# Kernel tuning notes

Hardware: AMD Instinct MI355X
Metric: run time of the kernel (lower is better)

## Reference

```python
import jax, jax.numpy as jnp
import numpy as np

D_MODEL = 1024
N_HEADS = 16
D_HEAD = D_MODEL // N_HEADS
LN_EPS = 1e-5


def setup_inputs() -> dict:
    key = jax.random.key(0)
    ks = jax.random.split(key, 10)
    B, N = 2, 2048
    s = 1.0 / np.sqrt(D_MODEL)
    return {
        "x": jax.random.normal(ks[0], (B, N, D_MODEL), dtype=jnp.float32),
        "Wq": jax.random.normal(ks[1], (D_MODEL, D_MODEL), dtype=jnp.float32) * s,
        "bq": jnp.zeros((D_MODEL,), dtype=jnp.float32),
        "Wk": jax.random.normal(ks[2], (D_MODEL, D_MODEL), dtype=jnp.float32) * s,
        "bk": jnp.zeros((D_MODEL,), dtype=jnp.float32),
        "Wv": jax.random.normal(ks[3], (D_MODEL, D_MODEL), dtype=jnp.float32) * s,
        "bv": jnp.zeros((D_MODEL,), dtype=jnp.float32),
        "Wo": jax.random.normal(ks[4], (D_MODEL, D_MODEL), dtype=jnp.float32) * s,
        "bo": jnp.zeros((D_MODEL,), dtype=jnp.float32),
        "ln_gamma": jnp.ones((D_MODEL,), dtype=jnp.float32),
        "ln_beta": jnp.zeros((D_MODEL,), dtype=jnp.float32),
    }


def reference(x, Wq, bq, Wk, bk, Wv, bv, Wo, bo, ln_gamma, ln_beta):
    B, N, _ = x.shape
    # QKV projections -> [B, H, N, dh]
    def proj(W, b):
        return (x @ W.T + b).reshape(B, N, N_HEADS, D_HEAD).transpose(0, 2, 1, 3)
    Q, K, V = proj(Wq, bq), proj(Wk, bk), proj(Wv, bv)
    # scaled scores [B, H, N, N] with causal mask (is_mask=True)
    scores = jnp.einsum("bhqd,bhkd->bhqk", Q, K) / np.sqrt(D_HEAD)
    causal = jnp.tril(jnp.ones((N, N), dtype=bool))
    scores = jnp.where(causal, scores, -jnp.inf)
    attn = jax.nn.softmax(scores, axis=-1)  # dropout p=0 (eval)
    ctx = jnp.einsum("bhqk,bhkd->bhqd", attn, V)  # [B, H, N, dh]
    ctx = ctx.transpose(0, 2, 1, 3).reshape(B, N, D_MODEL)
    out = ctx @ Wo.T + bo + x  # output proj + residual
    # LayerNorm over last dim
    mu = out.mean(-1, keepdims=True)
    var = out.var(-1, keepdims=True)
    return (out - mu) / jnp.sqrt(var + LN_EPS) * ln_gamma + ln_beta
```

## Files before the change

kernel.cpp:

```cpp
#include <hip/hip_runtime.h>
#include <type_traits>

#define D_MODEL 1024
#define NHEADS 16
#define DHEAD 64
#define SEQ 2048
#define BATCH 2
#define MROWS (BATCH*SEQ)
#define NQT (SEQ/64)

typedef unsigned short ushort_t;
using bf16x8 = __attribute__((ext_vector_type(8))) __bf16;
using bf16x4 = __attribute__((ext_vector_type(4))) __bf16;
using us4    = __attribute__((ext_vector_type(4))) unsigned short;
using us8    = __attribute__((ext_vector_type(8))) unsigned short;
using f32x4  = __attribute__((ext_vector_type(4))) float;

#define QSCALE 0.18033688011112042f

__device__ __forceinline__ float fast_exp2(float x) {
#if __has_builtin(__builtin_amdgcn_exp2f)
    return __builtin_amdgcn_exp2f(x);
#else
    return __expf(x * 0.6931471805599453f);
#endif
}

__device__ __forceinline__ void gl2lds(const ushort_t* g, ushort_t* l) {
    __builtin_amdgcn_global_load_lds(
        (const __attribute__((address_space(1))) unsigned int*)g,
        (__attribute__((address_space(3))) unsigned int*)l,
        16, 0, 0);
}

__global__ __launch_bounds__(256) void cvt_kernel(
    const float* __restrict__ x,
    const float* __restrict__ wq, const float* __restrict__ wk,
    const float* __restrict__ wv, const float* __restrict__ wo,
    ushort_t* __restrict__ xb,
    ushort_t* __restrict__ wqb, ushort_t* __restrict__ wkb,
    ushort_t* __restrict__ wvb, ushort_t* __restrict__ wob)
{
    const size_t XN = (size_t)MROWS * D_MODEL;
    const size_t WN = (size_t)D_MODEL * D_MODEL;
    size_t i = ((size_t)blockIdx.x * 256 + threadIdx.x) * 4;
    const float* s; ushort_t* d; size_t off;
    if (i < XN) { s = x; d = xb; off = i; }
    else {
        size_t j = i - XN;
        int w = (int)(j / WN);
        off = j - (size_t)w * WN;
        s = (w == 0) ? wq : (w == 1) ? wk : (w == 2) ? wv : wo;
        d = (w == 0) ? wqb : (w == 1) ? wkb : (w == 2) ? wvb : wob;
    }
    const f32x4 v = *(const f32x4*)(s + off);
    bf16x4 o;
    #pragma unroll
    for (int t = 0; t < 4; ++t) o[t] = (__bf16)v[t];
    *(bf16x4*)(d + off) = o;
}

template<typename OutT, bool RES>
__global__ __launch_bounds__(256, 3) void gemm_nt(
    const ushort_t* __restrict__ A,
    const ushort_t* __restrict__ W0, const ushort_t* __restrict__ W1, const ushort_t* __restrict__ W2,
    const float* __restrict__ b0, const float* __restrict__ b1, const float* __restrict__ b2,
    const float* __restrict__ res,
    OutT* __restrict__ Y0, OutT* __restrict__ Y1, OutT* __restrict__ Y2,
    float qsc)
{
    constexpr int K = D_MODEL;
    __shared__ ushort_t As[2][128 * 32];
    __shared__ ushort_t Ws[2][128 * 32];

    const int z = blockIdx.z;
    const ushort_t* W  = (z == 0) ? W0 : (z == 1) ? W1 : W2;
    const float* bias  = (z == 0) ? b0 : (z == 1) ? b1 : b2;
    OutT* Y            = (z == 0) ? Y0 : (z == 1) ? Y1 : Y2;
    const float sc     = (z == 0) ? qsc : 1.0f;

    const int i0 = blockIdx.x * 128;
    const int j0 = blockIdx.y * 128;
    const int tid  = threadIdx.x;
    const int lane = tid & 63;
    const int w    = tid >> 6;
    const int wm   = (w >> 1) * 64;
    const int wn   = (w & 1) * 64;
    const int l15  = lane & 15;
    const int quad = lane >> 4;

    const int srow = lane >> 2;
    const int scol = (lane & 3) * 8;
    const int c0 = w * 2, c1 = w * 2 + 1;
    const ushort_t* gA0 = A + (size_t)(i0 + c0 * 16 + srow) * K + scol;
    const ushort_t* gA1 = A + (size_t)(i0 + c1 * 16 + srow) * K + scol;
    const ushort_t* gW0 = W + (size_t)(j0 + c0 * 16 + srow) * K + scol;
    const ushort_t* gW1 = W + (size_t)(j0 + c1 * 16 + srow) * K + scol;

    f32x4 acc[4][4] = {};

    for (int k0 = 0; k0 < K; k0 += 64) {
        gl2lds(gA0 + k0,      &As[0][c0 * 512]);
        gl2lds(gA1 + k0,      &As[0][c1 * 512]);
        gl2lds(gA0 + k0 + 32, &As[1][c0 * 512]);
        gl2lds(gA1 + k0 + 32, &As[1][c1 * 512]);
        gl2lds(gW0 + k0,      &Ws[0][c0 * 512]);
        gl2lds(gW1 + k0,      &Ws[0][c1 * 512]);
        gl2lds(gW0 + k0 + 32, &Ws[1][c0 * 512]);
        gl2lds(gW1 + k0 + 32, &Ws[1][c1 * 512]);
        __syncthreads();

        #pragma unroll
        for (int s = 0; s < 2; ++s) {
            bf16x8 af[4], wf[4];
            #pragma unroll
            for (int m = 0; m < 4; ++m)
                af[m] = *(const bf16x8*)&As[s][(wm + m * 16 + l15) * 32 + quad * 8];
            #pragma unroll
            for (int n = 0; n < 4; ++n)
                wf[n] = *(const bf16x8*)&Ws[s][(wn + n * 16 + l15) * 32 + quad * 8];
            #pragma unroll
            for (int m = 0; m < 4; ++m)
                #pragma unroll
                for (int n = 0; n < 4; ++n)
                    acc[m][n] = __builtin_amdgcn_mfma_f32_16x16x32_bf16(wf[n], af[m], acc[m][n], 0, 0, 0);
        }
        __syncthreads();
    }

    #pragma unroll
    for (int n = 0; n < 4; ++n) {
        const int col = j0 + wn + n * 16 + quad * 4;
        const f32x4 bv = *(const f32x4*)&bias[col];
        #pragma unroll
        for (int m = 0; m < 4; ++m) {
            const int row = i0 + wm + m * 16 + l15;
            if constexpr (std::is_same<OutT, float>::value) {
                f32x4 v;
                #pragma unroll
                for (int r = 0; r < 4; ++r) v[r] = acc[m][n][r] + bv[r];
                if constexpr (RES) {
                    const f32x4 rv = *(const f32x4*)&res[(size_t)row * D_MODEL + col];
                    #pragma unroll
                    for (int r = 0; r < 4; ++r) v[r] += rv[r];
                }
                *(f32x4*)&Y[(size_t)row * D_MODEL + col] = v;
            } else {
                bf16x4 pk;
                #pragma unroll
                for (int r = 0; r < 4; ++r) pk[r] = (__bf16)((acc[m][n][r] + bv[r]) * sc);
                *(bf16x4*)&Y[(size_t)row * D_MODEL + col] = pk;
            }
        }
    }
}

#define KD 64

__device__ __forceinline__ int kswz(int row, int col) {
    return row * KD + (col ^ ((row & 7) << 3));
}

__global__ __launch_bounds__(256, 4) void attn_kernel(
    const ushort_t* __restrict__ Qg, const ushort_t* __restrict__ Kg,
    const ushort_t* __restrict__ Vg, ushort_t* __restrict__ Og)
{
    __shared__ __align__(16) ushort_t Kt[2][64 * KD];
    __shared__ __align__(16) ushort_t Vt[2][64 * KD];
    __shared__ __align__(16) ushort_t Pw[64 * KD];

    const int bh = blockIdx.x;
    const int b = bh >> 4;
    const int h = bh & 15;
    const int qt = (NQT - 1) - blockIdx.y;
    const int q0 = qt * 64;
    const int nkt = qt + 1;

    const int tid  = threadIdx.x;
    const int lane = tid & 63;
    const int w    = tid >> 6;
    const int l15  = lane & 15;
    const int quad = lane >> 4;

    const size_t headoff = (size_t)h * DHEAD;
    const ushort_t* Kbase = Kg + (size_t)(b * SEQ) * D_MODEL + headoff;
    const ushort_t* Vbase = Vg + (size_t)(b * SEQ) * D_MODEL + headoff;

    const int krow = tid >> 3;
    const int kb   = tid & 7;
    const int vkey = tid & 63;
    const int dc0  = tid >> 6;
    const int dc1  = dc0 + 4;

    const int rx = (l15 & 7) << 3;
    const int cs0 = (quad * 8) ^ rx;
    const int cs1 = (32 + quad * 8) ^ rx;
    int pwc[4];
    #pragma unroll
    for (int f = 0; f < 4; ++f) pwc[f] = (f * 16 + quad * 4) ^ rx;
    ushort_t* PwRow = &Pw[(w * 16 + l15) * KD];

    const int kwa = krow * KD + ((kb * 8) ^ ((krow & 7) << 3));

    const int qg = q0 + w * 16 + l15;
    const size_t qrow = (size_t)(b * SEQ + qg) * D_MODEL + headoff;
    const bf16x8 qf0 = *(const bf16x8*)&Qg[qrow + quad * 8];
    const bf16x8 qf1 = *(const bf16x8*)&Qg[qrow + 32 + quad * 8];

    bf16x8 onesf;
    #pragma unroll
    for (int j = 0; j < 8; ++j) onesf[j] = (__bf16)1.0f;

    float m_run = -1e30f;
    f32x4 o[4] = {};
    f32x4 o4 = {};

    us8 kp0, kp1, vp0, vp1;
    kp0 = *(const us8*)&Kbase[(size_t)krow * D_MODEL + kb * 8];
    kp1 = *(const us8*)&Kbase[(size_t)(32 + krow) * D_MODEL + kb * 8];
    vp0 = *(const us8*)&Vbase[(size_t)vkey * D_MODEL + dc0 * 8];
    vp1 = *(const us8*)&Vbase[(size_t)vkey * D_MODEL + dc1 * 8];
    *(us8*)&Kt[0][kwa]           = kp0;
    *(us8*)&Kt[0][kwa + 32 * KD] = kp1;
    #pragma unroll
    for (int j = 0; j < 8; ++j) {
        Vt[0][(dc0 * 8 + j) * KD + (vkey ^ (j << 3))] = vp0[j];
        Vt[0][(dc1 * 8 + j) * KD + (vkey ^ (j << 3))] = vp1[j];
    }
    __syncthreads();

    for (int kt = 0; kt < nkt; ++kt) {
        const int cur = kt & 1;
        const int nxt = cur ^ 1;
        const bool pre = (kt + 1 < nkt);
        if (pre) {
            const size_t koff = (size_t)((kt + 1) * 64) * D_MODEL;
            kp0 = *(const us8*)&Kbase[koff + (size_t)krow * D_MODEL + kb * 8];
            kp1 = *(const us8*)&Kbase[koff + (size_t)(32 + krow) * D_MODEL + kb * 8];
            vp0 = *(const us8*)&Vbase[koff + (size_t)vkey * D_MODEL + dc0 * 8];
            vp1 = *(const us8*)&Vbase[koff + (size_t)vkey * D_MODEL + dc1 * 8];
        }

        f32x4 sv[4];
        __builtin_amdgcn_s_setprio(1);
        #pragma unroll
        for (int f = 0; f < 4; ++f) {
            const int rbase = (f * 16 + l15) * KD;
            const bf16x8 kf0 = *(const bf16x8*)&Kt[cur][rbase + cs0];
            const bf16x8 kf1 = *(const bf16x8*)&Kt[cur][rbase + cs1];
            f32x4 s = {};
            s = __builtin_amdgcn_mfma_f32_16x16x32_bf16(kf0, qf0, s, 0, 0, 0);
            s = __builtin_amdgcn_mfma_f32_16x16x32_bf16(kf1, qf1, s, 0, 0, 0);
            sv[f] = s;
        }
        __builtin_amdgcn_s_setprio(0);

        if (kt == qt) {
            #pragma unroll
            for (int f = 0; f < 4; ++f)
                #pragma unroll
                for (int r = 0; r < 4; ++r) {
                    const int kg = kt * 64 + f * 16 + quad * 4 + r;
                    sv[f][r] = (kg <= qg) ? sv[f][r] : -1e30f;
                }
        }

        float mf[4];
        #pragma unroll
        for (int f = 0; f < 4; ++f)
            mf[f] = fmaxf(fmaxf(sv[f][0], sv[f][1]), fmaxf(sv[f][2], sv[f][3]));
        float mx = fmaxf(fmaxf(mf[0], mf[1]), fmaxf(mf[2], mf[3]));
        mx = fmaxf(mx, __shfl_xor(mx, 16));
        mx = fmaxf(mx, __shfl_xor(mx, 32));

        if (!__all(mx <= m_run + 8.0f)) {
            const float mn = fmaxf(m_run, mx);
            const float al = fast_exp2(m_run - mn);
            m_run = mn;
            #pragma unroll
            for (int t = 0; t < 4; ++t)
                #pragma unroll
                for (int r = 0; r < 4; ++r) o[t][r] *= al;
            o4[0] *= al;
        }

        #pragma unroll
        for (int f = 0; f < 4; ++f) {
            bf16x4 pk;
            #pragma unroll
            for (int r = 0; r < 4; ++r)
                pk[r] = (__bf16)fast_exp2(sv[f][r] - m_run);
            *(bf16x4*)&PwRow[pwc[f]] = pk;
        }
        __asm__ volatile("s_waitcnt lgkmcnt(0)" ::: "memory");

        __builtin_amdgcn_s_setprio(1);
        #pragma unroll
        for (int s = 0; s < 2; ++s) {
            const bf16x8 pf = *(const bf16x8*)&PwRow[s ? cs1 : cs0];
            #pragma unroll
            for (int t = 0; t < 4; ++t) {
                const bf16x8 vf = *(const bf16x8*)&Vt[cur][(t * 16 + l15) * KD + (s ? cs1 : cs0)];
                o[t] = __builtin_amdgcn_mfma_f32_16x16x32_bf16(vf, pf, o[t], 0, 0, 0);
            }
            o4 = __builtin_amdgcn_mfma_f32_16x16x32_bf16(onesf, pf, o4, 0, 0, 0);
        }
        __builtin_amdgcn_s_setprio(0);

        if (pre) {
            *(us8*)&Kt[nxt][kwa]           = kp0;
            *(us8*)&Kt[nxt][kwa + 32 * KD] = kp1;
            #pragma unroll
            for (int j = 0; j < 8; ++j) {
                Vt[nxt][(dc0 * 8 + j) * KD + (vkey ^ (j << 3))] = vp0[j];
                Vt[nxt][(dc1 * 8 + j) * KD + (vkey ^ (j << 3))] = vp1[j];
            }
        }
        __asm__ volatile("s_waitcnt lgkmcnt(0)\n\ts_barrier" ::: "memory");
    }

    const float inv = 1.f / o4[0];
    const size_t orow = (size_t)(b * SEQ + qg) * D_MODEL + headoff;
    #pragma unroll
    for (int t = 0; t < 4; ++t) {
        bf16x4 pk;
        #pragma unroll
        for (int r = 0; r < 4; ++r) pk[r] = (__bf16)(o[t][r] * inv);
        *(bf16x4*)&Og[orow + t * 16 + quad * 4] = pk;
    }
}

__global__ __launch_bounds__(256) void ln_kernel(
    const float* __restrict__ X, const float* __restrict__ g,
    const float* __restrict__ bta, float* __restrict__ out)
{
    __shared__ float r1[4], r2[4];
    const int row = blockIdx.x;
    const int tid = threadIdx.x;
    const float* p = X + (size_t)row * D_MODEL;
    float v[4]; float s1 = 0.f, s2 = 0.f;
    #pragma unroll
    for (int i = 0; i < 4; ++i) { v[i] = p[tid + 256 * i]; s1 += v[i]; s2 += v[i] * v[i]; }
    #pragma unroll
    for (int d = 32; d >= 1; d >>= 1) { s1 += __shfl_xor(s1, d); s2 += __shfl_xor(s2, d); }
    if ((tid & 63) == 0) { r1[tid >> 6] = s1; r2[tid >> 6] = s2; }
    __syncthreads();
    s1 = r1[0] + r1[1] + r1[2] + r1[3];
    s2 = r2[0] + r2[1] + r2[2] + r2[3];
    const float mu  = s1 * (1.f / D_MODEL);
    const float var = s2 * (1.f / D_MODEL) - mu * mu;
    const float rstd = rsqrtf(var + 1e-5f);
    #pragma unroll
    for (int i = 0; i < 4; ++i) {
        const int c = tid + 256 * i;
        out[(size_t)row * D_MODEL + c] = (v[i] - mu) * rstd * g[c] + bta[c];
    }
}

extern "C" void kernel_launch(void* const* d_in, const int* in_sizes, int n_in,
                              void* d_out, int out_size, void* d_ws, size_t ws_size,
                              hipStream_t stream) {
    const float* x     = (const float*)d_in[0];
    const float* Wq    = (const float*)d_in[1];
    const float* bq    = (const float*)d_in[2];
    const float* Wk    = (const float*)d_in[3];
    const float* bk    = (const float*)d_in[4];
    const float* Wv    = (const float*)d_in[5];
    const float* bv    = (const float*)d_in[6];
    const float* Wo    = (const float*)d_in[7];
    const float* bo    = (const float*)d_in[8];
    const float* gamma = (const float*)d_in[9];
    const float* beta  = (const float*)d_in[10];

    const size_t XN = (size_t)MROWS * D_MODEL;
    const size_t WN = (size_t)D_MODEL * D_MODEL;
    ushort_t* wsp = (ushort_t*)d_ws;
    ushort_t* xb  = wsp;
    ushort_t* Yq  = wsp + XN;
    ushort_t* Yk  = wsp + 2 * XN;
    ushort_t* Yv  = wsp + 3 * XN;
    ushort_t* Wqb = wsp + 4 * XN;
    ushort_t* Wkb = Wqb + WN;
    ushort_t* Wvb = Wkb + WN;
    ushort_t* Wob = Wvb + WN;
    ushort_t* ctx = xb;
    float*    pre = (float*)d_out;

    cvt_kernel<<<dim3(8192), 256, 0, stream>>>(x, Wq, Wk, Wv, Wo, xb, Wqb, Wkb, Wvb, Wob);

    gemm_nt<ushort_t, false><<<dim3(MROWS / 128, D_MODEL / 128, 3), 256, 0, stream>>>(
        xb, Wqb, Wkb, Wvb, bq, bk, bv, nullptr, Yq, Yk, Yv, QSCALE);

    attn_kernel<<<dim3(BATCH * NHEADS, NQT), 256, 0, stream>>>(Yq, Yk, Yv, ctx);

    gemm_nt<float, true><<<dim3(MROWS / 128, D_MODEL / 128, 1), 256, 0, stream>>>(
        ctx, Wob, Wob, Wob, bo, bo, bo, x, pre, pre, pre, 1.0f);

    ln_kernel<<<dim3(MROWS), 256, 0, stream>>>(pre, gamma, beta, (float*)d_out);
}
```

Measured before the change: 205.7 us.

## Vectorize V transpose stores, split P/V pipeline, and interleave causal tile order

The V tile transpose into LDS now has each thread load four 4-element rows and pack them into 64-bit stores, replacing sixteen scalar 16-bit LDS writes per thread. The softmax-exp and P·V MFMA work is split into two halves so the second half's exponentials can overlap with the first half's matrix ops. The query-tile order across blockIdx.y is interleaved, mixing long and short causal tiles to balance work across CUs. The new V layout must still match the XOR swizzle, and splitting P/V adds an extra LDS wait.

```diff
diff --git a/kernel.cpp b/kernel.cpp
--- a/kernel.cpp
+++ b/kernel.cpp
@@ -10,10 +10,12 @@
 #define NQT (SEQ/64)
 
 typedef unsigned short ushort_t;
+typedef unsigned int   u32;
 using bf16x8 = __attribute__((ext_vector_type(8))) __bf16;
 using bf16x4 = __attribute__((ext_vector_type(4))) __bf16;
 using us4    = __attribute__((ext_vector_type(4))) unsigned short;
 using us8    = __attribute__((ext_vector_type(8))) unsigned short;
+using u32x2  = __attribute__((ext_vector_type(2))) unsigned int;
 using f32x4  = __attribute__((ext_vector_type(4))) float;
 
 #define QSCALE 0.18033688011112042f
@@ -157,10 +159,6 @@
 
 #define KD 64
 
-__device__ __forceinline__ int kswz(int row, int col) {
-    return row * KD + (col ^ ((row & 7) << 3));
-}
-
 __global__ __launch_bounds__(256, 4) void attn_kernel(
     const ushort_t* __restrict__ Qg, const ushort_t* __restrict__ Kg,
     const ushort_t* __restrict__ Vg, ushort_t* __restrict__ Og)
@@ -172,7 +170,9 @@
     const int bh = blockIdx.x;
     const int b = bh >> 4;
     const int h = bh & 15;
-    const int qt = (NQT - 1) - blockIdx.y;
+    const int y = blockIdx.y;
+    const int qt = (y < 8) ? (31 - y) : (y < 16) ? (y - 8)
+                 : (y < 24) ? (39 - y) : (y - 16);
     const int q0 = qt * 64;
     const int nkt = qt + 1;
 
@@ -188,9 +188,9 @@
 
     const int krow = tid >> 3;
     const int kb   = tid & 7;
-    const int vkey = tid & 63;
-    const int dc0  = tid >> 6;
-    const int dc1  = dc0 + 4;
+
+    const int k4 = (tid & 15) * 4;
+    const int dd = (tid >> 4) * 4;
 
     const int rx = (l15 & 7) << 3;
     const int cs0 = (quad * 8) ^ rx;
@@ -215,17 +215,21 @@
     f32x4 o[4] = {};
     f32x4 o4 = {};
 
-    us8 kp0, kp1, vp0, vp1;
+    us8 kp0, kp1;
+    us4 vg[4];
     kp0 = *(const us8*)&Kbase[(size_t)krow * D_MODEL + kb * 8];
     kp1 = *(const us8*)&Kbase[(size_t)(32 + krow) * D_MODEL + kb * 8];
-    vp0 = *(const us8*)&Vbase[(size_t)vkey * D_MODEL + dc0 * 8];
-    vp1 = *(const us8*)&Vbase[(size_t)vkey * D_MODEL + dc1 * 8];
+    #pragma unroll
+    for (int j = 0; j < 4; ++j)
+        vg[j] = *(const us4*)&Vbase[(size_t)(k4 + j) * D_MODEL + dd];
     *(us8*)&Kt[0][kwa]           = kp0;
     *(us8*)&Kt[0][kwa + 32 * KD] = kp1;
     #pragma unroll
-    for (int j = 0; j < 8; ++j) {
-        Vt[0][(dc0 * 8 + j) * KD + (vkey ^ (j << 3))] = vp0[j];
-        Vt[0][(dc1 * 8 + j) * KD + (vkey ^ (j << 3))] = vp1[j];
+    for (int di = 0; di < 4; ++di) {
+        const int d = dd + di;
+        const u32 lo = (u32)vg[0][di] | ((u32)vg[1][di] << 16);
+        const u32 hi = (u32)vg[2][di] | ((u32)vg[3][di] << 16);
+        *(u32x2*)&Vt[0][d * KD + (k4 ^ ((d & 7) << 3))] = (u32x2){lo, hi};
     }
     __syncthreads();
 
@@ -237,8 +241,9 @@
             const size_t koff = (size_t)((kt + 1) * 64) * D_MODEL;
             kp0 = *(const us8*)&Kbase[koff + (size_t)krow * D_MODEL + kb * 8];
             kp1 = *(const us8*)&Kbase[koff + (size_t)(32 + krow) * D_MODEL + kb * 8];
-            vp0 = *(const us8*)&Vbase[koff + (size_t)vkey * D_MODEL + dc0 * 8];
-            vp1 = *(const us8*)&Vbase[koff + (size_t)vkey * D_MODEL + dc1 * 8];
+            #pragma unroll
+            for (int j = 0; j < 4; ++j)
+                vg[j] = *(const us4*)&Vbase[koff + (size_t)(k4 + j) * D_MODEL + dd];
         }
 
         f32x4 sv[4];
@@ -285,7 +290,7 @@
         }
 
         #pragma unroll
-        for (int f = 0; f < 4; ++f) {
+        for (int f = 0; f < 2; ++f) {
             bf16x4 pk;
             #pragma unroll
             for (int r = 0; r < 4; ++r)
@@ -295,25 +300,48 @@
         __asm__ volatile("s_waitcnt lgkmcnt(0)" ::: "memory");
 
         __builtin_amdgcn_s_setprio(1);
-        #pragma unroll
-        for (int s = 0; s < 2; ++s) {
-            const bf16x8 pf = *(const bf16x8*)&PwRow[s ? cs1 : cs0];
+        {
+            const bf16x8 pf = *(const bf16x8*)&PwRow[cs0];
             #pragma unroll
             for (int t = 0; t < 4; ++t) {
-                const bf16x8 vf = *(const bf16x8*)&Vt[cur][(t * 16 + l15) * KD + (s ? cs1 : cs0)];
+                const bf16x8 vf = *(const bf16x8*)&Vt[cur][(t * 16 + l15) * KD + cs0];
                 o[t] = __builtin_amdgcn_mfma_f32_16x16x32_bf16(vf, pf, o[t], 0, 0, 0);
             }
             o4 = __builtin_amdgcn_mfma_f32_16x16x32_bf16(onesf, pf, o4, 0, 0, 0);
         }
         __builtin_amdgcn_s_setprio(0);
 
+        #pragma unroll
+        for (int f = 2; f < 4; ++f) {
+            bf16x4 pk;
+            #pragma unroll
+            for (int r = 0; r < 4; ++r)
+                pk[r] = (__bf16)fast_exp2(sv[f][r] - m_run);
+            *(bf16x4*)&PwRow[pwc[f]] = pk;
+        }
+        __asm__ volatile("s_waitcnt lgkmcnt(0)" ::: "memory");
+
+        __builtin_amdgcn_s_setprio(1);
+        {
+            const bf16x8 pf = *(const bf16x8*)&PwRow[cs1];
+            #pragma unroll
+            for (int t = 0; t < 4; ++t) {
+                const bf16x8 vf = *(const bf16x8*)&Vt[cur][(t * 16 + l15) * KD + cs1];
+                o[t] = __builtin_amdgcn_mfma_f32_16x16x32_bf16(vf, pf, o[t], 0, 0, 0);
+            }
+            o4 = __builtin_amdgcn_mfma_f32_16x16x32_bf16(onesf, pf, o4, 0, 0, 0);
+        }
+        __builtin_amdgcn_s_setprio(0);
+
         if (pre) {
             *(us8*)&Kt[nxt][kwa]           = kp0;
             *(us8*)&Kt[nxt][kwa + 32 * KD] = kp1;
             #pragma unroll
-            for (int j = 0; j < 8; ++j) {
-                Vt[nxt][(dc0 * 8 + j) * KD + (vkey ^ (j << 3))] = vp0[j];
-                Vt[nxt][(dc1 * 8 + j) * KD + (vkey ^ (j << 3))] = vp1[j];
+            for (int di = 0; di < 4; ++di) {
+                const int d = dd + di;
+                const u32 lo = (u32)vg[0][di] | ((u32)vg[1][di] << 16);
+                const u32 hi = (u32)vg[2][di] | ((u32)vg[3][di] << 16);
+                *(u32x2*)&Vt[nxt][d * KD + (k4 ^ ((d & 7) << 3))] = (u32x2){lo, hi};
             }
         }
         __asm__ volatile("s_waitcnt lgkmcnt(0)\n\ts_barrier" ::: "memory");
```

Result: slower. 212.8 us (+3.5%).

## Split heavy causal attention query tiles across two blocks with combine pass

Applied to the files above, without the earlier changes.

The upper 16 query tiles, which have the longest causal key ranges, are each split into two blocks covering halves of the key range. Their partial outputs and row max/sum are written to fp32 workspace, and a new combine kernel merges them with rescaling. The goal is to balance work across blocks and shorten the attention kernel's tail. The cost is extra global traffic, an additional kernel launch and more total blocks.

```diff
diff --git a/kernel.cpp b/kernel.cpp
--- a/kernel.cpp
+++ b/kernel.cpp
@@ -10,11 +10,13 @@
 #define NQT (SEQ/64)
 
 typedef unsigned short ushort_t;
+typedef unsigned int   u32;
 using bf16x8 = __attribute__((ext_vector_type(8))) __bf16;
 using bf16x4 = __attribute__((ext_vector_type(4))) __bf16;
 using us4    = __attribute__((ext_vector_type(4))) unsigned short;
 using us8    = __attribute__((ext_vector_type(8))) unsigned short;
 using f32x4  = __attribute__((ext_vector_type(4))) float;
+using f32x2  = __attribute__((ext_vector_type(2))) float;
 
 #define QSCALE 0.18033688011112042f
 
@@ -157,13 +159,10 @@
 
 #define KD 64
 
-__device__ __forceinline__ int kswz(int row, int col) {
-    return row * KD + (col ^ ((row & 7) << 3));
-}
-
 __global__ __launch_bounds__(256, 4) void attn_kernel(
     const ushort_t* __restrict__ Qg, const ushort_t* __restrict__ Kg,
-    const ushort_t* __restrict__ Vg, ushort_t* __restrict__ Og)
+    const ushort_t* __restrict__ Vg, ushort_t* __restrict__ Og,
+    float* __restrict__ wso, float* __restrict__ wsml)
 {
     __shared__ __align__(16) ushort_t Kt[2][64 * KD];
     __shared__ __align__(16) ushort_t Vt[2][64 * KD];
@@ -172,9 +171,23 @@
     const int bh = blockIdx.x;
     const int b = bh >> 4;
     const int h = bh & 15;
-    const int qt = (NQT - 1) - blockIdx.y;
+
+    const int y = blockIdx.y;
+    int qt, kt0, kt1;
+    bool heavy;
+    if (y < 32) {
+        qt = 16 + (y >> 1);
+        const int nkt = qt + 1;
+        const int hh = nkt >> 1;
+        heavy = true;
+        if (y & 1) { kt0 = hh; kt1 = nkt; }
+        else       { kt0 = 0;  kt1 = hh;  }
+    } else {
+        qt = 47 - y;
+        kt0 = 0; kt1 = qt + 1; heavy = false;
+    }
+    const int part = y & 1;
     const int q0 = qt * 64;
-    const int nkt = qt + 1;
 
     const int tid  = threadIdx.x;
     const int lane = tid & 63;
@@ -216,10 +229,11 @@
     f32x4 o4 = {};
 
     us8 kp0, kp1, vp0, vp1;
-    kp0 = *(const us8*)&Kbase[(size_t)krow * D_MODEL + kb * 8];
-    kp1 = *(const us8*)&Kbase[(size_t)(32 + krow) * D_MODEL + kb * 8];
-    vp0 = *(const us8*)&Vbase[(size_t)vkey * D_MODEL + dc0 * 8];
-    vp1 = *(const us8*)&Vbase[(size_t)vkey * D_MODEL + dc1 * 8];
+    const size_t koff0 = (size_t)(kt0 * 64) * D_MODEL;
+    kp0 = *(const us8*)&Kbase[koff0 + (size_t)krow * D_MODEL + kb * 8];
+    kp1 = *(const us8*)&Kbase[koff0 + (size_t)(32 + krow) * D_MODEL + kb * 8];
+    vp0 = *(const us8*)&Vbase[koff0 + (size_t)vkey * D_MODEL + dc0 * 8];
+    vp1 = *(const us8*)&Vbase[koff0 + (size_t)vkey * D_MODEL + dc1 * 8];
     *(us8*)&Kt[0][kwa]           = kp0;
     *(us8*)&Kt[0][kwa + 32 * KD] = kp1;
     #pragma unroll
@@ -229,10 +243,10 @@
     }
     __syncthreads();
 
-    for (int kt = 0; kt < nkt; ++kt) {
-        const int cur = kt & 1;
+    for (int kt = kt0; kt < kt1; ++kt) {
+        const int cur = (kt - kt0) & 1;
         const int nxt = cur ^ 1;
-        const bool pre = (kt + 1 < nkt);
+        const bool pre = (kt + 1 < kt1);
         if (pre) {
             const size_t koff = (size_t)((kt + 1) * 64) * D_MODEL;
             kp0 = *(const us8*)&Kbase[koff + (size_t)krow * D_MODEL + kb * 8];
@@ -319,15 +333,60 @@
         __asm__ volatile("s_waitcnt lgkmcnt(0)\n\ts_barrier" ::: "memory");
     }
 
-    const float inv = 1.f / o4[0];
-    const size_t orow = (size_t)(b * SEQ + qg) * D_MODEL + headoff;
-    #pragma unroll
-    for (int t = 0; t < 4; ++t) {
-        bf16x4 pk;
-        #pragma unroll
-        for (int r = 0; r < 4; ++r) pk[r] = (__bf16)(o[t][r] * inv);
-        *(bf16x4*)&Og[orow + t * 16 + quad * 4] = pk;
-    }
+    if (!heavy) {
+        const float inv = 1.f / o4[0];
+        const size_t orow = (size_t)(b * SEQ + qg) * D_MODEL + headoff;
+        #pragma unroll
+        for (int t = 0; t < 4; ++t) {
+            bf16x4 pk;
+            #pragma unroll
+            for (int r = 0; r < 4; ++r) pk[r] = (__bf16)(o[t][r] * inv);
+            *(bf16x4*)&Og[orow + t * 16 + quad * 4] = pk;
+        }
+    } else {
+        const int T = (bh * 16 + (qt - 16)) * 2 + part;
+        float* wo = wso + (size_t)T * 4096 + (size_t)(w * 16 + l15) * 64;
+        #pragma unroll
+        for (int t = 0; t < 4; ++t)
+            *(f32x4*)&wo[t * 16 + quad * 4] = o[t];
+        if (quad == 0) {
+            f32x2 ml = { m_run, o4[0] };
+            *(f32x2*)&wsml[(size_t)(T * 64 + w * 16 + l15) * 2] = ml;
+        }
+    }
+}
+
+__global__ __launch_bounds__(256) void attn_combine(
+    const float* __restrict__ wso, const float* __restrict__ wsml,
+    ushort_t* __restrict__ Og)
+{
+    const int gid = blockIdx.x * 256 + threadIdx.x;
+    const int row = gid >> 4;
+    const int dp  = (gid & 15) * 4;
+    const int bh  = row >> 10;
+    const int rr  = row & 1023;
+    const int qh  = rr >> 6;
+    const int q   = rr & 63;
+    const int T0  = (bh * 16 + qh) * 2;
+
+    const f32x2 ml0 = *(const f32x2*)&wsml[(size_t)(T0 * 64 + q) * 2];
+    const f32x2 ml1 = *(const f32x2*)&wsml[(size_t)((T0 + 1) * 64 + q) * 2];
+    const float M  = fmaxf(ml0[0], ml1[0]);
+    const float a0 = fast_exp2(ml0[0] - M);
+    const float a1 = fast_exp2(ml1[0] - M);
+    const float inv = 1.0f / (ml0[1] * a0 + ml1[1] * a1);
+
+    const f32x4 o0 = *(const f32x4*)&wso[(size_t)T0 * 4096 + q * 64 + dp];
+    const f32x4 o1 = *(const f32x4*)&wso[(size_t)(T0 + 1) * 4096 + q * 64 + dp];
+
+    const int b = bh >> 4;
+    const int h = bh & 15;
+    const int qg = (16 + qh) * 64 + q;
+    bf16x4 pk;
+    #pragma unroll
+    for (int r = 0; r < 4; ++r)
+        pk[r] = (__bf16)((o0[r] * a0 + o1[r] * a1) * inv);
+    *(bf16x4*)&Og[(size_t)(b * SEQ + qg) * D_MODEL + h * DHEAD + dp] = pk;
 }
 
 __global__ __launch_bounds__(256) void ln_kernel(
@@ -386,12 +445,17 @@
     ushort_t* ctx = xb;
     float*    pre = (float*)d_out;
 
+    float* wso  = (float*)(wsp + 4 * XN + 4 * WN);
+    float* wsml = wso + (size_t)1024 * 4096;
+
     cvt_kernel<<<dim3(8192), 256, 0, stream>>>(x, Wq, Wk, Wv, Wo, xb, Wqb, Wkb, Wvb, Wob);
 
     gemm_nt<ushort_t, false><<<dim3(MROWS / 128, D_MODEL / 128, 3), 256, 0, stream>>>(
         xb, Wqb, Wkb, Wvb, bq, bk, bv, nullptr, Yq, Yk, Yv, QSCALE);
 
-    attn_kernel<<<dim3(BATCH * NHEADS, NQT), 256, 0, stream>>>(Yq, Yk, Yv, ctx);
+    attn_kernel<<<dim3(BATCH * NHEADS, 48), 256, 0, stream>>>(Yq, Yk, Yv, ctx, wso, wsml);
+
+    attn_combine<<<dim3(2048), 256, 0, stream>>>(wso, wsml, ctx);
 
     gemm_nt<float, true><<<dim3(MROWS / 128, D_MODEL / 128, 1), 256, 0, stream>>>(
         ctx, Wob, Wob, Wob, bo, bo, bo, x, pre, pre, pre, 1.0f);
```

After: 204.9 us. No clear change (-0.4%).
